# Kernel optimization log

Hardware: AMD Instinct MI355X
Metric: run time of the kernel (lower is better)

The kernel has to match this reference:

```python
import jax, jax.numpy as jnp
import numpy as np

N_SAMPLES = 8_000_000
NB_CLASSES = 5


def setup_inputs() -> dict:
    key = jax.random.key(0)
    k1, k2 = jax.random.split(key)
    preds = jax.random.normal(k1, (N_SAMPLES, NB_CLASSES), dtype=jnp.float32)
    true = jax.random.randint(k2, (N_SAMPLES,), 0, NB_CLASSES, dtype=jnp.int32)
    return {"preds": preds, "true": true}


def reference(preds, true):
    N, C = preds.shape
    dt = preds.dtype
    cls = jnp.arange(C, dtype=dt)

    # SoftArgmax1D per row (base_index=0, step_size=1), then round -> hard class
    soft_arg = jax.nn.softmax(preds, axis=1) @ cls            # [N]
    pred_idx = jnp.clip(jnp.round(soft_arg).astype(jnp.int32), 0, C - 1)

    # confusion_matrix[true, pred] += 1 via fused scatter-add on flat index
    flat = true * C + pred_idx                                 # [N]
    conf = jnp.zeros((C * C,), dtype=dt).at[flat].add(1.0).reshape(C, C)

    # quadratic kappa weights: (i-j)^2 / (C-1)^2
    weights = (cls[:, None] - cls[None, :]) ** 2 / ((C - 1) ** 2)

    # class histograms (scatter-add)
    true_hist = jnp.zeros((C,), dtype=dt).at[true].add(1.0)
    pred_hist = jnp.zeros((C,), dtype=dt).at[pred_idx].add(1.0)

    # expected matrix E = outer(true_hist, pred_hist), both normalized
    E = jnp.outer(true_hist, pred_hist)
    E = E / E.sum()
    conf = conf / conf.sum()

    num = (conf * weights).sum()
    den = (E * weights).sum()
    return num / den
```

## Files before the change

### kernel.cpp

```cpp
#include <hip/hip_runtime.h>
#include <math.h>

#define NCLS 5
#define NBINS 25
#define BIN_STRIDE 16
#define NBLOCKS 4096
#define NTHREADS 256

struct __attribute__((packed, aligned(4))) f4u { float x, y, z, w; };

__global__ void kappa_init(unsigned int* __restrict__ gbins) {
    int i = threadIdx.x;
    if (i < NBINS * BIN_STRIDE) gbins[i] = 0u;
}

__global__ void __launch_bounds__(NTHREADS)
kappa_count(const float* __restrict__ preds,
            const int* __restrict__ truev,
            int N,
            unsigned int* __restrict__ gbins) {
    __shared__ unsigned int s_conf[NBINS];
    const int tid = threadIdx.x;
    if (tid < NBINS) s_conf[tid] = 0u;
    __syncthreads();

    const int gstride = gridDim.x * blockDim.x;
    for (int i = blockIdx.x * blockDim.x + tid; i < N; i += gstride) {
        f4u v = *(const f4u*)(preds + (size_t)i * 5u);
        float v4 = preds[(size_t)i * 5u + 4u];
        int t = truev[i];

        float e0 = __expf(v.x);
        float e1 = __expf(v.y);
        float e2 = __expf(v.z);
        float e3 = __expf(v.w);
        float e4 = __expf(v4);
        float s   = e0 + e1 + e2 + e3 + e4;
        float dot = e1 + 2.f * e2 + 3.f * e3 + 4.f * e4;

        int pi = (int)rintf(dot / s);
        pi = min(max(pi, 0), NCLS - 1);
        atomicAdd(&s_conf[t * NCLS + pi], 1u);
    }

    __syncthreads();
    if (tid < NBINS) atomicAdd(&gbins[tid * BIN_STRIDE], s_conf[tid]);
}

__global__ void kappa_final(const unsigned int* __restrict__ gbins,
                            float* __restrict__ out) {
    __shared__ unsigned int s_conf[NBINS];
    const int tid = threadIdx.x;
    if (tid < NBINS) s_conf[tid] = gbins[tid * BIN_STRIDE];
    __syncthreads();

    if (tid == 0) {
        double conf[NBINS];
        double tot = 0.0;
        for (int i = 0; i < NBINS; i++) { conf[i] = (double)s_conf[i]; tot += conf[i]; }
        double th[NCLS] = {0, 0, 0, 0, 0};
        double ph[NCLS] = {0, 0, 0, 0, 0};
        for (int i = 0; i < NCLS; i++)
            for (int j = 0; j < NCLS; j++) {
                th[i] += conf[i * NCLS + j];
                ph[j] += conf[i * NCLS + j];
            }
        double num = 0.0, den = 0.0;
        for (int i = 0; i < NCLS; i++)
            for (int j = 0; j < NCLS; j++) {
                double w = (double)((i - j) * (i - j)) / 16.0;
                num += w * conf[i * NCLS + j];
                den += w * th[i] * ph[j];
            }
        out[0] = (float)(num * tot / den);
    }
}

extern "C" void kernel_launch(void* const* d_in, const int* in_sizes, int n_in,
                              void* d_out, int out_size, void* d_ws, size_t ws_size,
                              hipStream_t stream) {
    const float* preds = (const float*)d_in[0];
    const int* truev = (const int*)d_in[1];
    const int N = in_sizes[1];

    unsigned int* gbins = (unsigned int*)d_ws;

    kappa_init<<<1, 512, 0, stream>>>(gbins);
    kappa_count<<<NBLOCKS, NTHREADS, 0, stream>>>(preds, truev, N, gbins);
    kappa_final<<<1, 64, 0, stream>>>(gbins, (float*)d_out);
}
```

Before: 278.9 us.

## Stage prediction rows through shared memory with coalesced float4 loads

Replaces per-thread unaligned 20-byte row loads with block-wide coalesced float4 loads of 1024-row tiles (and int4 loads of labels) into shared memory, then computes the soft-argmax from LDS. Grid size is halved since each block now processes tiles. This aims to fix poor global memory coalescing, at the cost of extra LDS traffic and two barriers per tile. Tail label handling assumes N divisible by 4.

Result: faster. 266.5 us (-4.5%).

```diff
diff --git a/kernel.cpp b/kernel.cpp
--- a/kernel.cpp
+++ b/kernel.cpp
@@ -4,10 +4,9 @@
 #define NCLS 5
 #define NBINS 25
 #define BIN_STRIDE 16
-#define NBLOCKS 4096
+#define NBLOCKS 2048
 #define NTHREADS 256
-
-struct __attribute__((packed, aligned(4))) f4u { float x, y, z, w; };
+#define STAGE_ROWS 1024
 
 __global__ void kappa_init(unsigned int* __restrict__ gbins) {
     int i = threadIdx.x;
@@ -19,31 +18,56 @@
             const int* __restrict__ truev,
             int N,
             unsigned int* __restrict__ gbins) {
+    __shared__ float s_p[STAGE_ROWS * NCLS];
+    __shared__ int s_t[STAGE_ROWS];
     __shared__ unsigned int s_conf[NBINS];
+
     const int tid = threadIdx.x;
     if (tid < NBINS) s_conf[tid] = 0u;
-    __syncthreads();
 
-    const int gstride = gridDim.x * blockDim.x;
-    for (int i = blockIdx.x * blockDim.x + tid; i < N; i += gstride) {
-        f4u v = *(const f4u*)(preds + (size_t)i * 5u);
-        float v4 = preds[(size_t)i * 5u + 4u];
-        int t = truev[i];
+    const long total4 = ((long)N * NCLS) >> 2;
+    const int n4 = N >> 2;
+    const int nstages = (N + STAGE_ROWS - 1) / STAGE_ROWS;
 
-        float e0 = __expf(v.x);
-        float e1 = __expf(v.y);
-        float e2 = __expf(v.z);
-        float e3 = __expf(v.w);
-        float e4 = __expf(v4);
-        float s   = e0 + e1 + e2 + e3 + e4;
-        float dot = e1 + 2.f * e2 + 3.f * e3 + 4.f * e4;
+    for (int s = blockIdx.x; s < nstages; s += gridDim.x) {
+        const long row0 = (long)s * STAGE_ROWS;
+        const long f40 = row0 * NCLS / 4;
 
-        int pi = (int)rintf(dot / s);
-        pi = min(max(pi, 0), NCLS - 1);
-        atomicAdd(&s_conf[t * NCLS + pi], 1u);
+        const float4* __restrict__ p4 = (const float4*)preds;
+        #pragma unroll
+        for (int k = 0; k < 5; k++) {
+            int li = tid + (k << 8);
+            long g = f40 + li;
+            float4 v = (g < total4) ? p4[g] : float4{0.f, 0.f, 0.f, 0.f};
+            ((float4*)s_p)[li] = v;
+        }
+        {
+            long g = (row0 >> 2) + tid;
+            int4 tv = (g < n4) ? ((const int4*)truev)[g] : int4{0, 0, 0, 0};
+            ((int4*)s_t)[tid] = tv;
+        }
+        __syncthreads();
+
+        #pragma unroll
+        for (int k = 0; k < 4; k++) {
+            int r = tid + (k << 8);
+            if (row0 + r < N) {
+                const float* rp = s_p + r * NCLS;
+                float e0 = __expf(rp[0]);
+                float e1 = __expf(rp[1]);
+                float e2 = __expf(rp[2]);
+                float e3 = __expf(rp[3]);
+                float e4 = __expf(rp[4]);
+                float ssum = e0 + e1 + e2 + e3 + e4;
+                float dot = e1 + 2.f * e2 + 3.f * e3 + 4.f * e4;
+                int pi = (int)rintf(dot / ssum);
+                pi = min(max(pi, 0), NCLS - 1);
+                atomicAdd(&s_conf[s_t[r] * NCLS + pi], 1u);
+            }
+        }
+        __syncthreads();
     }
 
-    __syncthreads();
     if (tid < NBINS) atomicAdd(&gbins[tid * BIN_STRIDE], s_conf[tid]);
 }
 
```
